# Optimization experiments

Measured on AMD Instinct MI355X. Metric: run time of the kernel, lower is better.

## Reference

```python
import jax, jax.numpy as jnp
import numpy as np

B, T, V, E, H = 128, 512, 32000, 512, 2048


def setup_inputs() -> dict:
    key = jax.random.key(0)
    ks = jax.random.split(key, 10)
    s = lambda k, shape: jax.random.normal(k, shape, dtype=jnp.float32) * 0.02
    return {
        "input_ids": jax.random.randint(ks[0], (B, T), 0, V),
        "emb": s(ks[1], (V, E)),
        # layer 0: embed_size -> hidden_size
        "Wih0": s(ks[2], (H, E)), "Whh0": s(ks[3], (H, H)),
        "bih0": jnp.zeros((H,), jnp.float32), "bhh0": jnp.zeros((H,), jnp.float32),
        # layer 1: hidden_size -> hidden_size
        "Wih1": s(ks[4], (H, H)), "Whh1": s(ks[5], (H, H)),
        "bih1": jnp.zeros((H,), jnp.float32), "bhh1": jnp.zeros((H,), jnp.float32),
        # head: Linear(H,E) -> ReLU -> Linear(E,V)
        "W1": s(ks[6], (E, H)), "b1": jnp.zeros((E,), jnp.float32),
        "W2": s(ks[7], (V, E)), "b2": jnp.zeros((V,), jnp.float32),
    }


def reference(input_ids, emb, Wih0, Whh0, bih0, bhh0, Wih1, Whh1, bih1, bhh1, W1, b1, W2, b2):
    # embedding lookup for whole sequence, then scan over time
    xs = jnp.swapaxes(emb[input_ids], 0, 1)  # [T, B, E]
    b = input_ids.shape[0]
    h_init = (jnp.zeros((b, Whh0.shape[0]), xs.dtype),
              jnp.zeros((b, Whh1.shape[0]), xs.dtype))

    def step(carry, x_t):
        h0, h1 = carry
        h0 = jnp.tanh(x_t @ Wih0.T + bih0 + h0 @ Whh0.T + bhh0)
        h1 = jnp.tanh(h0 @ Wih1.T + bih1 + h1 @ Whh1.T + bhh1)
        return (h0, h1), None

    (_, h1), _ = jax.lax.scan(step, h_init, xs)
    # MLP head on final top-layer hidden state only
    return jnp.maximum(h1 @ W1.T + b1, 0.0) @ W2.T + b2  # [B, V]
```

## Files before the change

kernel.cpp:

```cpp
#include <hip/hip_runtime.h>
#include <hip/hip_bf16.h>
#include <stdint.h>

#define Bn 128
#define Tn 512
#define En 512
#define Hn 2048
#define Vn 32000
#define R0 8
#define R1 4
#define HSLOT (Bn*Hn)

typedef float f32x4 __attribute__((ext_vector_type(4)));
typedef short bf16x8 __attribute__((ext_vector_type(8)));
typedef unsigned long long u64;

__device__ __forceinline__ unsigned short f2b(float f) {
  uint32_t x = __builtin_bit_cast(uint32_t, f);
  uint32_t r = x + 0x7FFFu + ((x >> 16) & 1u);
  return (unsigned short)(r >> 16);
}

union U16x8 { bf16x8 v; u64 q[2]; };
union F32x4u { f32x4 v; u64 q[2]; };

__device__ __forceinline__ bf16x8 ld_h(const unsigned short* p) {
  U16x8 u;
  u.q[0] = __hip_atomic_load((const u64*)p,     __ATOMIC_RELAXED, __HIP_MEMORY_SCOPE_AGENT);
  u.q[1] = __hip_atomic_load((const u64*)p + 1, __ATOMIC_RELAXED, __HIP_MEMORY_SCOPE_AGENT);
  return u.v;
}
__device__ __forceinline__ f32x4 ld_p(const float* p) {
  F32x4u u;
  u.q[0] = __hip_atomic_load((const u64*)p,     __ATOMIC_RELAXED, __HIP_MEMORY_SCOPE_AGENT);
  u.q[1] = __hip_atomic_load((const u64*)p + 1, __ATOMIC_RELAXED, __HIP_MEMORY_SCOPE_AGENT);
  return u.v;
}
__device__ __forceinline__ void st_p(float* p, f32x4 x) {
  F32x4u u; u.v = x;
  __hip_atomic_store((u64*)p,     u.q[0], __ATOMIC_RELAXED, __HIP_MEMORY_SCOPE_AGENT);
  __hip_atomic_store((u64*)p + 1, u.q[1], __ATOMIC_RELAXED, __HIP_MEMORY_SCOPE_AGENT);
}
__device__ __forceinline__ uint32_t ldf(const uint32_t* p) {
  return __hip_atomic_load(p, __ATOMIC_RELAXED, __HIP_MEMORY_SCOPE_AGENT);
}
__device__ __forceinline__ void stf(uint32_t* p, uint32_t v) {
  __hip_atomic_store(p, v, __ATOMIC_RELAXED, __HIP_MEMORY_SCOPE_AGENT);
}
__device__ __forceinline__ void drain_then_sync() {
  asm volatile("s_waitcnt vmcnt(0)" ::: "memory");
  __syncthreads();
}

#define NREP 8
#define FA_PART_BASE 8192
#define FB_PART_BASE 9216
#define FLAG_WORDS 16384


__global__ void zero3(uint32_t* a, int na, uint32_t* b, int nb, uint32_t* c, int nc) {
  int i = blockIdx.x * 256 + threadIdx.x;
  if (i < na) a[i] = 0u;
  if (i < nb) b[i] = 0u;
  if (i < nc) c[i] = 0u;
}

__global__ void pack_bias(const float* bih0, const float* bhh0,
                          const float* bih1, const float* bhh1,
                          float* bias0, float* bias1) {
  int i = blockIdx.x * 256 + threadIdx.x;
  bias0[i] = bih0[i] + bhh0[i];
  bias1[i] = bih1[i] + bhh1[i];
}

__global__ void pack_imgA(const float* __restrict__ Wih0, const float* __restrict__ Whh0,
                          uint4* __restrict__ imgA) {
  int tid = blockIdx.x * 256 + threadIdx.x;
  int wg = tid / 5120;
  int p  = tid - wg * 5120;
  int l = p & 63;
  int ckt = p >> 6;
  int ct = ckt & 3, kt = ckt >> 2;
  int g = wg >> 2, s = wg & 3;
  int col = g * 64 + ct * 16 + (l & 15);
  int kv0 = s * 640 + kt * 32 + (l >> 4) * 8;
  const float* src = (kv0 < 512) ? (Wih0 + (size_t)col * En + kv0)
                                 : (Whh0 + (size_t)col * Hn + (kv0 - 512));
  unsigned short o[8];
#pragma unroll
  for (int j = 0; j < 8; ++j) o[j] = f2b(src[j]);
  imgA[tid] = *reinterpret_cast<uint4*>(o);
}

__global__ void pack_imgB(const float* __restrict__ Wih1, const float* __restrict__ Whh1,
                          uint4* __restrict__ imgB) {
  int tid = blockIdx.x * 256 + threadIdx.x;
  int wg = tid >> 13;
  int p  = tid & 8191;
  int l = p & 63;
  int ckt = p >> 6;
  int ct = ckt & 3, kt = ckt >> 2;
  int g = wg >> 2, s = wg & 3;
  int col = g * 64 + ct * 16 + (l & 15);
  int kv0 = s * 1024 + kt * 32 + (l >> 4) * 8;
  const float* src = (kv0 < 2048) ? (Wih1 + (size_t)col * Hn + kv0)
                                  : (Whh1 + (size_t)col * Hn + (kv0 - 2048));
  unsigned short o[8];
#pragma unroll
  for (int j = 0; j < 8; ++j) o[j] = f2b(src[j]);
  imgB[tid] = *reinterpret_cast<uint4*>(o);
}

__global__ void pack_imgW1(const float* __restrict__ W1, uint4* __restrict__ img) {
  int tid = blockIdx.x * 256 + threadIdx.x;
  int grp = tid >> 12;
  int p = tid & 4095;
  int l = p & 63;
  int kt = p >> 6;
  int col = grp * 16 + (l & 15);
  int k0 = kt * 32 + (l >> 4) * 8;
  const float* src = W1 + (size_t)col * Hn + k0;
  unsigned short o[8];
#pragma unroll
  for (int j = 0; j < 8; ++j) o[j] = f2b(src[j]);
  img[tid] = *reinterpret_cast<uint4*>(o);
}

__global__ void pack_imgW2(const float* __restrict__ W2, uint4* __restrict__ img) {
  int tid = blockIdx.x * 256 + threadIdx.x;
  int grp = tid >> 12;
  int p = tid & 4095;
  int l = p & 63;
  int ckt = p >> 6;
  int ct = ckt & 3, kt = ckt >> 2;
  int col = grp * 64 + ct * 16 + (l & 15);
  int k0 = kt * 32 + (l >> 4) * 8;
  const float* src = W2 + (size_t)col * En + k0;
  unsigned short o[8];
#pragma unroll
  for (int j = 0; j < 8; ++j) o[j] = f2b(src[j]);
  img[tid] = *reinterpret_cast<uint4*>(o);
}

__global__ void gather_x(const int* __restrict__ ids, const float* __restrict__ emb,
                         uint4* __restrict__ xall) {
  int tid = blockIdx.x * 256 + threadIdx.x;
  int t = tid >> 13;
  int r = tid & 8191;
  int b = r >> 6;
  int e8 = r & 63;
  int id = ids[b * Tn + t];
  const float* src = emb + (size_t)id * En + e8 * 8;
  unsigned short o[8];
#pragma unroll
  for (int j = 0; j < 8; ++j) o[j] = f2b(src[j]);
  xall[tid] = *reinterpret_cast<uint4*>(o);
}

__global__ __launch_bounds__(256) void rnn_persist(
    const uint4* __restrict__ imgA, const uint4* __restrict__ imgB,
    const unsigned short* __restrict__ xall,
    unsigned short* __restrict__ h0ring, unsigned short* __restrict__ h1ring,
    float* __restrict__ pbufA, float* __restrict__ pbufB,
    const float* __restrict__ bias0, const float* __restrict__ bias1,
    uint32_t* flags) {
  __shared__ uint4 smem[8192];
  const int tid = threadIdx.x;
  const int w = tid >> 6;
  const int l = tid & 63;
  const int l15 = l & 15;
  const int kq = l >> 4;
  const int blk = blockIdx.x;
  const int myrep = blk & (NREP - 1);
  const uint32_t* fA0r = flags + (size_t)myrep * 1024;
  const uint32_t* fB0r = flags + (size_t)myrep * 1024 + 64;
  uint32_t* fApart = flags + FA_PART_BASE;
  uint32_t* fBpart = flags + FB_PART_BASE;

  const bool roleA = (blk < 128);
  {
    const uint4* src = roleA ? (imgA + (size_t)blk * 5120) : (imgB + (size_t)(blk - 128) * 8192);
    const int n = roleA ? 5120 : 8192;
    for (int i = tid; i < n; i += 256) smem[i] = src[i];
  }
  __syncthreads();
  const bf16x8* wlds = reinterpret_cast<const bf16x8*>(smem);
  const int row0 = w * 32 + l15;

  if (roleA) {
    const int g = blk >> 2, s = blk & 3;
    const int colbase = g * 64;
    for (int t = 0; t < Tn; ++t) {
      {
        const bool ring = (s == 0) && (t + 1 > R0);
        for (;;) {
          int ok = 1;
          if (tid < 32) ok = (ldf(&fA0r[tid]) >= (uint32_t)t);
          if (ring && tid >= 64 && tid < 96)
            ok &= (ldf(&fB0r[tid - 64]) >= (uint32_t)(t + 1 - R0));
          if (__syncthreads_and(ok)) break;
          __builtin_amdgcn_s_sleep(2);
        }
        __builtin_amdgcn_fence(__ATOMIC_ACQUIRE, "workgroup");
      }
      const unsigned short* h0prev = h0ring + (size_t)((t + R0 - 1) % R0) * HSLOT;
      const unsigned short* xt = xall + (size_t)t * (Bn * En);
      f32x4 acc[2][4];
#pragma unroll
      for (int mt = 0; mt < 2; ++mt)
#pragma unroll
        for (int ct = 0; ct < 4; ++ct) acc[mt][ct] = (f32x4){0.f, 0.f, 0.f, 0.f};
#pragma unroll 4
      for (int kt = 0; kt < 20; ++kt) {
        const int kv = s * 640 + kt * 32;
        bf16x8 af0, af1;
        if (kv < 512) {
          af0 = *reinterpret_cast<const bf16x8*>(xt + kv + (size_t)row0 * En + kq * 8);
          af1 = *reinterpret_cast<const bf16x8*>(xt + kv + (size_t)(row0 + 16) * En + kq * 8);
        } else {
          const unsigned short* hp = h0prev + (kv - 512);
          af0 = ld_h(hp + (size_t)row0 * Hn + kq * 8);
          af1 = ld_h(hp + (size_t)(row0 + 16) * Hn + kq * 8);
        }
#pragma unroll
        for (int ct = 0; ct < 4; ++ct) {
          bf16x8 bf = wlds[(kt * 4 + ct) * 64 + l];
          acc[0][ct] = __builtin_amdgcn_mfma_f32_16x16x32_bf16(af0, bf, acc[0][ct], 0, 0, 0);
          acc[1][ct] = __builtin_amdgcn_mfma_f32_16x16x32_bf16(af1, bf, acc[1][ct], 0, 0, 0);
        }
      }
      if (s != 0) {
        float* slot = pbufA + (size_t)blk * 8192;
#pragma unroll
        for (int mt = 0; mt < 2; ++mt)
#pragma unroll
          for (int ct = 0; ct < 4; ++ct)
            st_p(slot + ((w * 8 + mt * 4 + ct) * 256 + l * 4), acc[mt][ct]);
        drain_then_sync();
        if (tid == 0) stf(&fApart[g * 16 + s], (uint32_t)(t + 1));
      } else {
        for (;;) {
          int ok = 1;
          if (tid < 3) ok = (ldf(&fApart[g * 16 + 1 + tid]) >= (uint32_t)(t + 1));
          if (__syncthreads_and(ok)) break;
          __builtin_amdgcn_s_sleep(2);
        }
        __builtin_amdgcn_fence(__ATOMIC_ACQUIRE, "workgroup");
        const float* p1 = pbufA + (size_t)(blk + 1) * 8192;
        const float* p2 = pbufA + (size_t)(blk + 2) * 8192;
        const float* p3 = pbufA + (size_t)(blk + 3) * 8192;
        unsigned short* h0cur = h0ring + (size_t)(t % R0) * HSLOT;
#pragma unroll
        for (int mt = 0; mt < 2; ++mt) {
#pragma unroll
          for (int ct = 0; ct < 4; ++ct) {
            const int base = (w * 8 + mt * 4 + ct) * 256 + l * 4;
            f32x4 sum = acc[mt][ct];
            sum += ld_p(p1 + base);
            sum += ld_p(p2 + base);
            sum += ld_p(p3 + base);
            const int col = colbase + ct * 16 + l15;
            const float bb = bias0[col];
#pragma unroll
            for (int r = 0; r < 4; ++r) {
              float v = tanhf(sum[r] + bb);
              int bo = f2b(v);
              int po = __shfl_down(bo, 1);
              if ((l15 & 1) == 0) {
                const int row = w * 32 + mt * 16 + kq * 4 + r;
                uint32_t packed = (uint32_t)(unsigned short)bo | ((uint32_t)(unsigned short)po << 16);
                stf((uint32_t*)(h0cur + (size_t)row * Hn + col), packed);
              }
            }
          }
        }
        drain_then_sync();
        if (tid < NREP) stf(flags + (size_t)tid * 1024 + g, (uint32_t)(t + 1));
      }
    }
  } else {
    const int bb = blk - 128;
    const int g = bb >> 2, s = bb & 3;
    const int colbase = g * 64;
    for (int t = 0; t < Tn; ++t) {
      {
        const bool ring = (s == 0) && (t + 2 > R1);
        for (;;) {
          int ok = 1;
          if (s < 2) {
            if (tid < 32) ok = (ldf(&fA0r[tid]) >= (uint32_t)(t + 1));
            if (s == 1 && t > 0 && tid == 33)
              ok &= (ldf(&fB0r[g]) >= (uint32_t)t);
          } else {
            if (tid < 32) ok = (ldf(&fB0r[tid]) >= (uint32_t)t);
          }
          if (ring && tid >= 64 && tid < 96)
            ok &= (ldf(&fB0r[tid - 64]) >= (uint32_t)(t + 2 - R1));
          if (__syncthreads_and(ok)) break;
          __builtin_amdgcn_s_sleep(2);
        }
        __builtin_amdgcn_fence(__ATOMIC_ACQUIRE, "workgroup");
      }
      const unsigned short* h0cur = h0ring + (size_t)(t % R0) * HSLOT;
      const unsigned short* h1prev = h1ring + (size_t)((t + R1 - 1) % R1) * HSLOT;
      const unsigned short* apbase;
      if (s == 0)      apbase = h0cur;
      else if (s == 1) apbase = h0cur + 1024;
      else if (s == 2) apbase = h1prev;
      else             apbase = h1prev + 1024;
      f32x4 acc[2][4];
#pragma unroll
      for (int mt = 0; mt < 2; ++mt)
#pragma unroll
        for (int ct = 0; ct < 4; ++ct) acc[mt][ct] = (f32x4){0.f, 0.f, 0.f, 0.f};
#pragma unroll 4
      for (int kt = 0; kt < 32; ++kt) {
        const unsigned short* ap = apbase + kt * 32;
        bf16x8 af0 = ld_h(ap + (size_t)row0 * Hn + kq * 8);
        bf16x8 af1 = ld_h(ap + (size_t)(row0 + 16) * Hn + kq * 8);
#pragma unroll
        for (int ct = 0; ct < 4; ++ct) {
          bf16x8 bf = wlds[(kt * 4 + ct) * 64 + l];
          acc[0][ct] = __builtin_amdgcn_mfma_f32_16x16x32_bf16(af0, bf, acc[0][ct], 0, 0, 0);
          acc[1][ct] = __builtin_amdgcn_mfma_f32_16x16x32_bf16(af1, bf, acc[1][ct], 0, 0, 0);
        }
      }
      if (s != 0) {
        float* slot = pbufB + (size_t)bb * 8192;
#pragma unroll
        for (int mt = 0; mt < 2; ++mt)
#pragma unroll
          for (int ct = 0; ct < 4; ++ct)
            st_p(slot + ((w * 8 + mt * 4 + ct) * 256 + l * 4), acc[mt][ct]);
        drain_then_sync();
        if (tid == 0) stf(&fBpart[g * 16 + s], (uint32_t)(t + 1));
      } else {
        for (;;) {
          int ok = 1;
          if (tid < 3) ok = (ldf(&fBpart[g * 16 + 1 + tid]) >= (uint32_t)(t + 1));
          if (__syncthreads_and(ok)) break;
          __builtin_amdgcn_s_sleep(2);
        }
        __builtin_amdgcn_fence(__ATOMIC_ACQUIRE, "workgroup");
        const float* p1 = pbufB + (size_t)(bb + 1) * 8192;
        const float* p2 = pbufB + (size_t)(bb + 2) * 8192;
        const float* p3 = pbufB + (size_t)(bb + 3) * 8192;
        unsigned short* h1cur = h1ring + (size_t)(t % R1) * HSLOT;
#pragma unroll
        for (int mt = 0; mt < 2; ++mt) {
#pragma unroll
          for (int ct = 0; ct < 4; ++ct) {
            const int base = (w * 8 + mt * 4 + ct) * 256 + l * 4;
            f32x4 sum = acc[mt][ct];
            sum += ld_p(p1 + base);
            sum += ld_p(p2 + base);
            sum += ld_p(p3 + base);
            const int col = colbase + ct * 16 + l15;
            const float bb2 = bias1[col];
#pragma unroll
            for (int r = 0; r < 4; ++r) {
              float v = tanhf(sum[r] + bb2);
              int bo = f2b(v);
              int po = __shfl_down(bo, 1);
              if ((l15 & 1) == 0) {
                const int row = w * 32 + mt * 16 + kq * 4 + r;
                uint32_t packed = (uint32_t)(unsigned short)bo | ((uint32_t)(unsigned short)po << 16);
                stf((uint32_t*)(h1cur + (size_t)row * Hn + col), packed);
              }
            }
          }
        }
        drain_then_sync();
        if (tid < NREP) stf(flags + (size_t)tid * 1024 + 64 + g, (uint32_t)(t + 1));
      }
    }
  }
}

__global__ __launch_bounds__(256) void head1(const uint4* __restrict__ imgW1,
                                             const unsigned short* __restrict__ h1f,
                                             const float* __restrict__ b1,
                                             unsigned short* __restrict__ a1) {
  __shared__ uint4 smem[4096];
  const int tid = threadIdx.x;
  const int w = tid >> 6, l = tid & 63, l15 = l & 15, kq = l >> 4;
  const int g = blockIdx.x;
  const uint4* src = imgW1 + (size_t)g * 4096;
  for (int i = tid; i < 4096; i += 256) smem[i] = src[i];
  __syncthreads();
  const bf16x8* wlds = reinterpret_cast<const bf16x8*>(smem);
  const int row0 = w * 32 + l15;
  f32x4 acc[2];
  acc[0] = (f32x4){0.f, 0.f, 0.f, 0.f};
  acc[1] = (f32x4){0.f, 0.f, 0.f, 0.f};
#pragma unroll 4
  for (int kt = 0; kt < 64; ++kt) {
    bf16x8 af0 = *reinterpret_cast<const bf16x8*>(h1f + (size_t)row0 * Hn + kt * 32 + kq * 8);
    bf16x8 af1 = *reinterpret_cast<const bf16x8*>(h1f + (size_t)(row0 + 16) * Hn + kt * 32 + kq * 8);
    bf16x8 bf = wlds[kt * 64 + l];
    acc[0] = __builtin_amdgcn_mfma_f32_16x16x32_bf16(af0, bf, acc[0], 0, 0, 0);
    acc[1] = __builtin_amdgcn_mfma_f32_16x16x32_bf16(af1, bf, acc[1], 0, 0, 0);
  }
  const int col = g * 16 + l15;
  const float bb = b1[col];
#pragma unroll
  for (int mt = 0; mt < 2; ++mt)
#pragma unroll
    for (int r = 0; r < 4; ++r) {
      float v = fmaxf(acc[mt][r] + bb, 0.f);
      const int row = w * 32 + mt * 16 + kq * 4 + r;
      a1[(size_t)row * En + col] = f2b(v);
    }
}

__global__ __launch_bounds__(256) void head2(const uint4* __restrict__ imgW2,
                                             const unsigned short* __restrict__ a1,
                                             const float* __restrict__ b2,
                                             float* __restrict__ out) {
  __shared__ uint4 smem[4096];
  const int tid = threadIdx.x;
  const int w = tid >> 6, l = tid & 63, l15 = l & 15, kq = l >> 4;
  const int g = blockIdx.x;
  const uint4* src = imgW2 + (size_t)g * 4096;
  for (int i = tid; i < 4096; i += 256) smem[i] = src[i];
  __syncthreads();
  const bf16x8* wlds = reinterpret_cast<const bf16x8*>(smem);
  const int row0 = w * 32 + l15;
  f32x4 acc[2][4];
#pragma unroll
  for (int mt = 0; mt < 2; ++mt)
#pragma unroll
    for (int ct = 0; ct < 4; ++ct) acc[mt][ct] = (f32x4){0.f, 0.f, 0.f, 0.f};
#pragma unroll
  for (int kt = 0; kt < 16; ++kt) {
    bf16x8 af0 = *reinterpret_cast<const bf16x8*>(a1 + (size_t)row0 * En + kt * 32 + kq * 8);
    bf16x8 af1 = *reinterpret_cast<const bf16x8*>(a1 + (size_t)(row0 + 16) * En + kt * 32 + kq * 8);
#pragma unroll
    for (int ct = 0; ct < 4; ++ct) {
      bf16x8 bf = wlds[(kt * 4 + ct) * 64 + l];
      acc[0][ct] = __builtin_amdgcn_mfma_f32_16x16x32_bf16(af0, bf, acc[0][ct], 0, 0, 0);
      acc[1][ct] = __builtin_amdgcn_mfma_f32_16x16x32_bf16(af1, bf, acc[1][ct], 0, 0, 0);
    }
  }
#pragma unroll
  for (int mt = 0; mt < 2; ++mt)
#pragma unroll
    for (int ct = 0; ct < 4; ++ct) {
      const int col = g * 64 + ct * 16 + l15;
      const float bb = b2[col];
#pragma unroll
      for (int r = 0; r < 4; ++r) {
        const int row = w * 32 + mt * 16 + kq * 4 + r;
        out[(size_t)row * Vn + col] = acc[mt][ct][r] + bb;
      }
    }
}

extern "C" void kernel_launch(void* const* d_in, const int* in_sizes, int n_in,
                              void* d_out, int out_size, void* d_ws, size_t ws_size,
                              hipStream_t stream) {
  (void)in_sizes; (void)n_in; (void)out_size;
  const int* ids    = (const int*)d_in[0];
  const float* emb  = (const float*)d_in[1];
  const float* Wih0 = (const float*)d_in[2];
  const float* Whh0 = (const float*)d_in[3];
  const float* bih0 = (const float*)d_in[4];
  const float* bhh0 = (const float*)d_in[5];
  const float* Wih1 = (const float*)d_in[6];
  const float* Whh1 = (const float*)d_in[7];
  const float* bih1 = (const float*)d_in[8];
  const float* bhh1 = (const float*)d_in[9];
  const float* W1   = (const float*)d_in[10];
  const float* b1   = (const float*)d_in[11];
  const float* W2   = (const float*)d_in[12];
  const float* b2   = (const float*)d_in[13];
  float* out = (float*)d_out;

  char* ws = (char*)d_ws;
  size_t o = 0;
  auto alloc = [&](size_t bytes) -> char* {
    char* p = ws + o;
    o += (bytes + 255) & ~(size_t)255;
    return p;
  };
  uint32_t* flags = (uint32_t*)alloc(FLAG_WORDS * 4);
  float* bias0 = (float*)alloc(Hn * 4);
  float* bias1 = (float*)alloc(Hn * 4);
  unsigned short* h0ring = (unsigned short*)alloc((size_t)R0 * HSLOT * 2);
  unsigned short* h1ring = (unsigned short*)alloc((size_t)R1 * HSLOT * 2);
  float* pbufA = (float*)alloc(128ull * 8192 * 4);
  float* pbufB = (float*)alloc(128ull * 8192 * 4);
  unsigned short* a1 = (unsigned short*)alloc((size_t)Bn * En * 2);
  uint4* imgA  = (uint4*)alloc(128ull * 5120 * 16);
  uint4* imgB  = (uint4*)alloc(128ull * 8192 * 16);
  uint4* imgW1 = (uint4*)alloc(32ull * 4096 * 16);
  uint4* imgW2 = (uint4*)alloc(500ull * 4096 * 16);
  uint4* xall  = (uint4*)alloc((size_t)Tn * Bn * En * 2);
  if (o > ws_size) return;

  zero3<<<512, 256, 0, stream>>>(flags, FLAG_WORDS,
                                 (uint32_t*)(h0ring + (size_t)(R0 - 1) * HSLOT), 131072,
                                 (uint32_t*)(h1ring + (size_t)(R1 - 1) * HSLOT), 131072);
  pack_bias<<<8, 256, 0, stream>>>(bih0, bhh0, bih1, bhh1, bias0, bias1);
  pack_imgA<<<2560, 256, 0, stream>>>(Wih0, Whh0, imgA);
  pack_imgB<<<4096, 256, 0, stream>>>(Wih1, Whh1, imgB);
  pack_imgW1<<<512, 256, 0, stream>>>(W1, imgW1);
  pack_imgW2<<<8000, 256, 0, stream>>>(W2, imgW2);
  gather_x<<<16384, 256, 0, stream>>>(ids, emb, xall);

  rnn_persist<<<256, 256, 0, stream>>>(imgA, imgB, (const unsigned short*)xall,
                                       h0ring, h1ring, pbufA, pbufB, bias0, bias1, flags);

  head1<<<32, 256, 0, stream>>>(imgW1, h1ring + (size_t)(511 % R1) * HSLOT, b1, a1);
  head2<<<500, 256, 0, stream>>>(imgW2, a1, b2, out);
}
```

Baseline: 14.10 ms.

## Split RNN into four weight roles with in-block K-split and off-critical-path input projections

The persistent RNN kernel is restructured into four roles of 64 blocks each (Whh0, Wih0, Wih1, Whh1), each owning 32 output columns with 512 threads. The two halves of each block split K and reduce through LDS instead of through cross-block partial buffers. The x·Wih0 and h1·Whh1 products are computed ahead of time by separate blocks into double-buffered partials, which shortens the serial dependency chain per timestep. Activation loads become batched inline-asm global loads with cache-bypass bits. The cost is more complex flag dependencies and a risk of deadlock or ordering bugs.

```diff
diff --git a/kernel.cpp b/kernel.cpp
--- a/kernel.cpp
+++ b/kernel.cpp
@@ -11,6 +11,10 @@
 #define R1 4
 #define HSLOT (Bn*Hn)
 
+#define NREP 8
+#define FXS 8192
+#define FLAG_WORDS 16384
+
 typedef float f32x4 __attribute__((ext_vector_type(4)));
 typedef short bf16x8 __attribute__((ext_vector_type(8)));
 typedef unsigned long long u64;
@@ -21,15 +25,7 @@
   return (unsigned short)(r >> 16);
 }
 
-union U16x8 { bf16x8 v; u64 q[2]; };
 union F32x4u { f32x4 v; u64 q[2]; };
-
-__device__ __forceinline__ bf16x8 ld_h(const unsigned short* p) {
-  U16x8 u;
-  u.q[0] = __hip_atomic_load((const u64*)p,     __ATOMIC_RELAXED, __HIP_MEMORY_SCOPE_AGENT);
-  u.q[1] = __hip_atomic_load((const u64*)p + 1, __ATOMIC_RELAXED, __HIP_MEMORY_SCOPE_AGENT);
-  return u.v;
-}
 __device__ __forceinline__ f32x4 ld_p(const float* p) {
   F32x4u u;
   u.q[0] = __hip_atomic_load((const u64*)p,     __ATOMIC_RELAXED, __HIP_MEMORY_SCOPE_AGENT);
@@ -51,11 +47,6 @@
   asm volatile("s_waitcnt vmcnt(0)" ::: "memory");
   __syncthreads();
 }
-
-#define NREP 8
-#define FA_PART_BASE 8192
-#define FB_PART_BASE 9216
-#define FLAG_WORDS 16384
 
 
 __global__ void zero3(uint32_t* a, int na, uint32_t* b, int nb, uint32_t* c, int nc) {
@@ -73,42 +64,19 @@
   bias1[i] = bih1[i] + bhh1[i];
 }
 
-__global__ void pack_imgA(const float* __restrict__ Wih0, const float* __restrict__ Whh0,
-                          uint4* __restrict__ imgA) {
+__global__ void pack_w32(const float* __restrict__ src, int Kd, uint4* __restrict__ img) {
   int tid = blockIdx.x * 256 + threadIdx.x;
-  int wg = tid / 5120;
-  int p  = tid - wg * 5120;
-  int l = p & 63;
-  int ckt = p >> 6;
-  int ct = ckt & 3, kt = ckt >> 2;
-  int g = wg >> 2, s = wg & 3;
-  int col = g * 64 + ct * 16 + (l & 15);
-  int kv0 = s * 640 + kt * 32 + (l >> 4) * 8;
-  const float* src = (kv0 < 512) ? (Wih0 + (size_t)col * En + kv0)
-                                 : (Whh0 + (size_t)col * Hn + (kv0 - 512));
+  int per = Kd * 4;
+  int g = tid / per, p = tid - g * per;
+  int l = p & 63, q = p >> 6;
+  int ct = q & 1, kt = q >> 1;
+  int col = g * 32 + ct * 16 + (l & 15);
+  int k0 = kt * 32 + (l >> 4) * 8;
+  const float* s = src + (size_t)col * Kd + k0;
   unsigned short o[8];
 #pragma unroll
-  for (int j = 0; j < 8; ++j) o[j] = f2b(src[j]);
-  imgA[tid] = *reinterpret_cast<uint4*>(o);
-}
-
-__global__ void pack_imgB(const float* __restrict__ Wih1, const float* __restrict__ Whh1,
-                          uint4* __restrict__ imgB) {
-  int tid = blockIdx.x * 256 + threadIdx.x;
-  int wg = tid >> 13;
-  int p  = tid & 8191;
-  int l = p & 63;
-  int ckt = p >> 6;
-  int ct = ckt & 3, kt = ckt >> 2;
-  int g = wg >> 2, s = wg & 3;
-  int col = g * 64 + ct * 16 + (l & 15);
-  int kv0 = s * 1024 + kt * 32 + (l >> 4) * 8;
-  const float* src = (kv0 < 2048) ? (Wih1 + (size_t)col * Hn + kv0)
-                                  : (Whh1 + (size_t)col * Hn + (kv0 - 2048));
-  unsigned short o[8];
-#pragma unroll
-  for (int j = 0; j < 8; ++j) o[j] = f2b(src[j]);
-  imgB[tid] = *reinterpret_cast<uint4*>(o);
+  for (int j = 0; j < 8; ++j) o[j] = f2b(s[j]);
+  img[tid] = *reinterpret_cast<uint4*>(o);
 }
 
 __global__ void pack_imgW1(const float* __restrict__ W1, uint4* __restrict__ img) {
@@ -157,223 +125,195 @@
   xall[tid] = *reinterpret_cast<uint4*>(o);
 }
 
-__global__ __launch_bounds__(256) void rnn_persist(
-    const uint4* __restrict__ imgA, const uint4* __restrict__ imgB,
+__global__ __launch_bounds__(512, 1) void rnn_persist(
+    const uint4* __restrict__ imgWhh0, const uint4* __restrict__ imgWih0,
+    const uint4* __restrict__ imgWih1, const uint4* __restrict__ imgWhh1,
     const unsigned short* __restrict__ xall,
     unsigned short* __restrict__ h0ring, unsigned short* __restrict__ h1ring,
-    float* __restrict__ pbufA, float* __restrict__ pbufB,
+    float* __restrict__ xpbuf, float* __restrict__ bpbuf,
     const float* __restrict__ bias0, const float* __restrict__ bias1,
     uint32_t* flags) {
   __shared__ uint4 smem[8192];
+  __shared__ f32x4 rbuf[1024];
   const int tid = threadIdx.x;
-  const int w = tid >> 6;
-  const int l = tid & 63;
-  const int l15 = l & 15;
-  const int kq = l >> 4;
+  const int w = tid >> 6, l = tid & 63, l15 = l & 15, kq = l >> 4;
+  const int wh = w & 3, half = w >> 2;
   const int blk = blockIdx.x;
+  const int role = blk >> 6, g = blk & 63;
   const int myrep = blk & (NREP - 1);
   const uint32_t* fA0r = flags + (size_t)myrep * 1024;
-  const uint32_t* fB0r = flags + (size_t)myrep * 1024 + 64;
-  uint32_t* fApart = flags + FA_PART_BASE;
-  uint32_t* fBpart = flags + FB_PART_BASE;
-
-  const bool roleA = (blk < 128);
-  {
-    const uint4* src = roleA ? (imgA + (size_t)blk * 5120) : (imgB + (size_t)(blk - 128) * 8192);
-    const int n = roleA ? 5120 : 8192;
-    for (int i = tid; i < n; i += 256) smem[i] = src[i];
-  }
+  const uint32_t* fB0r = flags + (size_t)myrep * 1024 + 128;
+  const uint32_t* fP1r = flags + (size_t)myrep * 1024 + 256;
+
+  const uint4* wsrc; int npkt, Kd;
+  if (role == 0)      { wsrc = imgWhh0 + (size_t)g * 8192; npkt = 8192; Kd = 2048; }
+  else if (role == 1) { wsrc = imgWih0 + (size_t)g * 2048; npkt = 2048; Kd = 512; }
+  else if (role == 2) { wsrc = imgWih1 + (size_t)g * 8192; npkt = 8192; Kd = 2048; }
+  else                { wsrc = imgWhh1 + (size_t)g * 8192; npkt = 8192; Kd = 2048; }
+  for (int i = tid; i < npkt; i += 512) smem[i] = wsrc[i];
   __syncthreads();
   const bf16x8* wlds = reinterpret_cast<const bf16x8*>(smem);
-  const int row0 = w * 32 + l15;
-
-  if (roleA) {
-    const int g = blk >> 2, s = blk & 3;
-    const int colbase = g * 64;
-    for (int t = 0; t < Tn; ++t) {
-      {
-        const bool ring = (s == 0) && (t + 1 > R0);
+  const int row0 = wh * 32 + l15;
+  const int nb = Kd >> 9;
+  const int khe = half * (Kd >> 1);
+  const int kt0 = khe >> 5;
+
+  for (int t = 0; t < Tn; ++t) {
+    if (role == 0) {
+      const bool ring = (t + 1 > R0);
+      for (;;) {
+        int ok = 1;
+        if (tid < 64) ok = (ldf(&fA0r[tid]) >= (uint32_t)t);
+        else if (tid == 64) ok = (ldf(flags + FXS + g * 16) >= (uint32_t)(t + 1));
+        else if (ring && tid >= 128 && tid < 192) ok = (ldf(&fB0r[tid - 128]) >= (uint32_t)(t + 1 - R0));
+        if (__syncthreads_and(ok)) break;
+        __builtin_amdgcn_s_sleep(1);
+      }
+    } else if (role == 1) {
+      if (t >= 2) {
         for (;;) {
           int ok = 1;
-          if (tid < 32) ok = (ldf(&fA0r[tid]) >= (uint32_t)t);
-          if (ring && tid >= 64 && tid < 96)
-            ok &= (ldf(&fB0r[tid - 64]) >= (uint32_t)(t + 1 - R0));
+          if (tid == 0) ok = (ldf(&fA0r[g]) >= (uint32_t)(t - 1));
           if (__syncthreads_and(ok)) break;
           __builtin_amdgcn_s_sleep(2);
         }
-        __builtin_amdgcn_fence(__ATOMIC_ACQUIRE, "workgroup");
-      }
-      const unsigned short* h0prev = h0ring + (size_t)((t + R0 - 1) % R0) * HSLOT;
-      const unsigned short* xt = xall + (size_t)t * (Bn * En);
-      f32x4 acc[2][4];
+      }
+    } else if (role == 2) {
+      const bool ring = (t + 2 > R1);
+      for (;;) {
+        int ok = 1;
+        if (tid < 64) ok = (ldf(&fA0r[tid]) >= (uint32_t)(t + 1));
+        else if (tid == 64) ok = (ldf(&fP1r[g]) >= (uint32_t)(t + 1));
+        else if (ring && tid >= 128 && tid < 192) ok = (ldf(&fP1r[tid - 128]) >= (uint32_t)(t + 2 - R1));
+        if (__syncthreads_and(ok)) break;
+        __builtin_amdgcn_s_sleep(1);
+      }
+    } else {
+      for (;;) {
+        int ok = 1;
+        if (tid < 64) ok = (ldf(&fB0r[tid]) >= (uint32_t)t);
+        if (__syncthreads_and(ok)) break;
+        __builtin_amdgcn_s_sleep(1);
+      }
+    }
+    __builtin_amdgcn_fence(__ATOMIC_ACQUIRE, "workgroup");
+
+    const unsigned short* asrc; int astride;
+    if (role == 0)      { asrc = h0ring + (size_t)((t + R0 - 1) % R0) * HSLOT; astride = Hn; }
+    else if (role == 1) { asrc = xall + (size_t)t * (Bn * En); astride = En; }
+    else if (role == 2) { asrc = h0ring + (size_t)(t % R0) * HSLOT; astride = Hn; }
+    else                { asrc = h1ring + (size_t)((t + R1 - 1) % R1) * HSLOT; astride = Hn; }
+
+    f32x4 acc[2][2];
+#pragma unroll
+    for (int mt = 0; mt < 2; ++mt)
+#pragma unroll
+      for (int ct = 0; ct < 2; ++ct) acc[mt][ct] = (f32x4){0.f, 0.f, 0.f, 0.f};
+
+    const unsigned short* pr0 = asrc + (size_t)row0 * astride + khe + kq * 8;
+    const unsigned short* pr1 = pr0 + (size_t)16 * astride;
+    for (int b = 0; b < nb; ++b) {
+      const unsigned short* pa = pr0 + b * 256;
+      const unsigned short* pb = pr1 + b * 256;
+      bf16x8 v0, v1, v2, v3, v4, v5, v6, v7, v8, v9, va, vb, vc, vd, ve, vf;
+      asm volatile(
+          "global_load_dwordx4 %[t0], %[a], off sc0 sc1\n\t"
+          "global_load_dwordx4 %[t1], %[a], off offset:64 sc0 sc1\n\t"
+          "global_load_dwordx4 %[t2], %[a], off offset:128 sc0 sc1\n\t"
+          "global_load_dwordx4 %[t3], %[a], off offset:192 sc0 sc1\n\t"
+          "global_load_dwordx4 %[t4], %[a], off offset:256 sc0 sc1\n\t"
+          "global_load_dwordx4 %[t5], %[a], off offset:320 sc0 sc1\n\t"
+          "global_load_dwordx4 %[t6], %[a], off offset:384 sc0 sc1\n\t"
+          "global_load_dwordx4 %[t7], %[a], off offset:448 sc0 sc1\n\t"
+          "global_load_dwordx4 %[t8], %[b], off sc0 sc1\n\t"
+          "global_load_dwordx4 %[t9], %[b], off offset:64 sc0 sc1\n\t"
+          "global_load_dwordx4 %[ta], %[b], off offset:128 sc0 sc1\n\t"
+          "global_load_dwordx4 %[tb], %[b], off offset:192 sc0 sc1\n\t"
+          "global_load_dwordx4 %[tc], %[b], off offset:256 sc0 sc1\n\t"
+          "global_load_dwordx4 %[td], %[b], off offset:320 sc0 sc1\n\t"
+          "global_load_dwordx4 %[te], %[b], off offset:384 sc0 sc1\n\t"
+          "global_load_dwordx4 %[tf], %[b], off offset:448 sc0 sc1\n\t"
+          "s_waitcnt vmcnt(0)"
+          : [t0]"=&v"(v0), [t1]"=&v"(v1), [t2]"=&v"(v2), [t3]"=&v"(v3),
+            [t4]"=&v"(v4), [t5]"=&v"(v5), [t6]"=&v"(v6), [t7]"=&v"(v7),
+            [t8]"=&v"(v8), [t9]"=&v"(v9), [ta]"=&v"(va), [tb]"=&v"(vb),
+            [tc]"=&v"(vc), [td]"=&v"(vd), [te]"=&v"(ve), [tf]"=&v"(vf)
+          : [a]"v"(pa), [b]"v"(pb)
+          : "memory");
+      __builtin_amdgcn_sched_barrier(0);
+      const int ktg = kt0 + b * 8;
+#define MFMA4(AF0, AF1, KT) do { \
+        bf16x8 bw0 = wlds[((KT) * 2) * 64 + l]; \
+        bf16x8 bw1 = wlds[((KT) * 2 + 1) * 64 + l]; \
+        acc[0][0] = __builtin_amdgcn_mfma_f32_16x16x32_bf16(AF0, bw0, acc[0][0], 0, 0, 0); \
+        acc[0][1] = __builtin_amdgcn_mfma_f32_16x16x32_bf16(AF0, bw1, acc[0][1], 0, 0, 0); \
+        acc[1][0] = __builtin_amdgcn_mfma_f32_16x16x32_bf16(AF1, bw0, acc[1][0], 0, 0, 0); \
+        acc[1][1] = __builtin_amdgcn_mfma_f32_16x16x32_bf16(AF1, bw1, acc[1][1], 0, 0, 0); \
+      } while (0)
+      MFMA4(v0, v8, ktg + 0); MFMA4(v1, v9, ktg + 1);
+      MFMA4(v2, va, ktg + 2); MFMA4(v3, vb, ktg + 3);
+      MFMA4(v4, vc, ktg + 4); MFMA4(v5, vd, ktg + 5);
+      MFMA4(v6, ve, ktg + 6); MFMA4(v7, vf, ktg + 7);
+#undef MFMA4
+    }
+
+    __syncthreads();
+    if (half == 1) {
 #pragma unroll
       for (int mt = 0; mt < 2; ++mt)
 #pragma unroll
-        for (int ct = 0; ct < 4; ++ct) acc[mt][ct] = (f32x4){0.f, 0.f, 0.f, 0.f};
-#pragma unroll 4
-      for (int kt = 0; kt < 20; ++kt) {
-        const int kv = s * 640 + kt * 32;
-        bf16x8 af0, af1;
-        if (kv < 512) {
-          af0 = *reinterpret_cast<const bf16x8*>(xt + kv + (size_t)row0 * En + kq * 8);
-          af1 = *reinterpret_cast<const bf16x8*>(xt + kv + (size_t)(row0 + 16) * En + kq * 8);
-        } else {
-          const unsigned short* hp = h0prev + (kv - 512);
-          af0 = ld_h(hp + (size_t)row0 * Hn + kq * 8);
-          af1 = ld_h(hp + (size_t)(row0 + 16) * Hn + kq * 8);
-        }
-#pragma unroll
-        for (int ct = 0; ct < 4; ++ct) {
-          bf16x8 bf = wlds[(kt * 4 + ct) * 64 + l];
-          acc[0][ct] = __builtin_amdgcn_mfma_f32_16x16x32_bf16(af0, bf, acc[0][ct], 0, 0, 0);
-          acc[1][ct] = __builtin_amdgcn_mfma_f32_16x16x32_bf16(af1, bf, acc[1][ct], 0, 0, 0);
-        }
-      }
-      if (s != 0) {
-        float* slot = pbufA + (size_t)blk * 8192;
-#pragma unroll
-        for (int mt = 0; mt < 2; ++mt)
-#pragma unroll
-          for (int ct = 0; ct < 4; ++ct)
-            st_p(slot + ((w * 8 + mt * 4 + ct) * 256 + l * 4), acc[mt][ct]);
-        drain_then_sync();
-        if (tid == 0) stf(&fApart[g * 16 + s], (uint32_t)(t + 1));
-      } else {
-        for (;;) {
-          int ok = 1;
-          if (tid < 3) ok = (ldf(&fApart[g * 16 + 1 + tid]) >= (uint32_t)(t + 1));
-          if (__syncthreads_and(ok)) break;
-          __builtin_amdgcn_s_sleep(2);
-        }
-        __builtin_amdgcn_fence(__ATOMIC_ACQUIRE, "workgroup");
-        const float* p1 = pbufA + (size_t)(blk + 1) * 8192;
-        const float* p2 = pbufA + (size_t)(blk + 2) * 8192;
-        const float* p3 = pbufA + (size_t)(blk + 3) * 8192;
-        unsigned short* h0cur = h0ring + (size_t)(t % R0) * HSLOT;
+        for (int ct = 0; ct < 2; ++ct)
+          rbuf[(wh * 4 + mt * 2 + ct) * 64 + l] = acc[mt][ct];
+    }
+    __syncthreads();
+
+    if (half == 0) {
+#pragma unroll
+      for (int mt = 0; mt < 2; ++mt)
+#pragma unroll
+        for (int ct = 0; ct < 2; ++ct)
+          acc[mt][ct] += rbuf[(wh * 4 + mt * 2 + ct) * 64 + l];
+
+      if (role == 0 || role == 2) {
+        const float* pb2 = (role == 0 ? xpbuf : bpbuf) + (size_t)(g * 2 + (t & 1)) * 4096;
+        const float* bsrc = (role == 0) ? bias0 : bias1;
+        unsigned short* hdst = (role == 0) ? (h0ring + (size_t)(t % R0) * HSLOT)
+                                           : (h1ring + (size_t)(t % R1) * HSLOT);
 #pragma unroll
         for (int mt = 0; mt < 2; ++mt) {
 #pragma unroll
-          for (int ct = 0; ct < 4; ++ct) {
-            const int base = (w * 8 + mt * 4 + ct) * 256 + l * 4;
-            f32x4 sum = acc[mt][ct];
-            sum += ld_p(p1 + base);
-            sum += ld_p(p2 + base);
-            sum += ld_p(p3 + base);
-            const int col = colbase + ct * 16 + l15;
-            const float bb = bias0[col];
+          for (int ct = 0; ct < 2; ++ct) {
+            const int idx = (wh * 4 + mt * 2 + ct) * 256 + l * 4;
+            f32x4 sum = acc[mt][ct] + ld_p(pb2 + idx);
+            const int col = g * 32 + ct * 16 + l15;
+            const float bb = bsrc[col];
 #pragma unroll
             for (int r = 0; r < 4; ++r) {
               float v = tanhf(sum[r] + bb);
               int bo = f2b(v);
               int po = __shfl_down(bo, 1);
               if ((l15 & 1) == 0) {
-                const int row = w * 32 + mt * 16 + kq * 4 + r;
+                const int row = wh * 32 + mt * 16 + kq * 4 + r;
                 uint32_t packed = (uint32_t)(unsigned short)bo | ((uint32_t)(unsigned short)po << 16);
-                stf((uint32_t*)(h0cur + (size_t)row * Hn + col), packed);
+                stf((uint32_t*)(hdst + (size_t)row * Hn + col), packed);
               }
             }
           }
         }
-        drain_then_sync();
-        if (tid < NREP) stf(flags + (size_t)tid * 1024 + g, (uint32_t)(t + 1));
-      }
-    }
-  } else {
-    const int bb = blk - 128;
-    const int g = bb >> 2, s = bb & 3;
-    const int colbase = g * 64;
-    for (int t = 0; t < Tn; ++t) {
-      {
-        const bool ring = (s == 0) && (t + 2 > R1);
-        for (;;) {
-          int ok = 1;
-          if (s < 2) {
-            if (tid < 32) ok = (ldf(&fA0r[tid]) >= (uint32_t)(t + 1));
-            if (s == 1 && t > 0 && tid == 33)
-              ok &= (ldf(&fB0r[g]) >= (uint32_t)t);
-          } else {
-            if (tid < 32) ok = (ldf(&fB0r[tid]) >= (uint32_t)t);
-          }
-          if (ring && tid >= 64 && tid < 96)
-            ok &= (ldf(&fB0r[tid - 64]) >= (uint32_t)(t + 2 - R1));
-          if (__syncthreads_and(ok)) break;
-          __builtin_amdgcn_s_sleep(2);
-        }
-        __builtin_amdgcn_fence(__ATOMIC_ACQUIRE, "workgroup");
-      }
-      const unsigned short* h0cur = h0ring + (size_t)(t % R0) * HSLOT;
-      const unsigned short* h1prev = h1ring + (size_t)((t + R1 - 1) % R1) * HSLOT;
-      const unsigned short* apbase;
-      if (s == 0)      apbase = h0cur;
-      else if (s == 1) apbase = h0cur + 1024;
-      else if (s == 2) apbase = h1prev;
-      else             apbase = h1prev + 1024;
-      f32x4 acc[2][4];
-#pragma unroll
-      for (int mt = 0; mt < 2; ++mt)
-#pragma unroll
-        for (int ct = 0; ct < 4; ++ct) acc[mt][ct] = (f32x4){0.f, 0.f, 0.f, 0.f};
-#pragma unroll 4
-      for (int kt = 0; kt < 32; ++kt) {
-        const unsigned short* ap = apbase + kt * 32;
-        bf16x8 af0 = ld_h(ap + (size_t)row0 * Hn + kq * 8);
-        bf16x8 af1 = ld_h(ap + (size_t)(row0 + 16) * Hn + kq * 8);
-#pragma unroll
-        for (int ct = 0; ct < 4; ++ct) {
-          bf16x8 bf = wlds[(kt * 4 + ct) * 64 + l];
-          acc[0][ct] = __builtin_amdgcn_mfma_f32_16x16x32_bf16(af0, bf, acc[0][ct], 0, 0, 0);
-          acc[1][ct] = __builtin_amdgcn_mfma_f32_16x16x32_bf16(af1, bf, acc[1][ct], 0, 0, 0);
-        }
-      }
-      if (s != 0) {
-        float* slot = pbufB + (size_t)bb * 8192;
+      } else {
+        float* dst = (role == 1 ? xpbuf : bpbuf) + (size_t)(g * 2 + (t & 1)) * 4096;
 #pragma unroll
         for (int mt = 0; mt < 2; ++mt)
 #pragma unroll
-          for (int ct = 0; ct < 4; ++ct)
-            st_p(slot + ((w * 8 + mt * 4 + ct) * 256 + l * 4), acc[mt][ct]);
-        drain_then_sync();
-        if (tid == 0) stf(&fBpart[g * 16 + s], (uint32_t)(t + 1));
-      } else {
-        for (;;) {
-          int ok = 1;
-          if (tid < 3) ok = (ldf(&fBpart[g * 16 + 1 + tid]) >= (uint32_t)(t + 1));
-          if (__syncthreads_and(ok)) break;
-          __builtin_amdgcn_s_sleep(2);
-        }
-        __builtin_amdgcn_fence(__ATOMIC_ACQUIRE, "workgroup");
-        const float* p1 = pbufB + (size_t)(bb + 1) * 8192;
-        const float* p2 = pbufB + (size_t)(bb + 2) * 8192;
-        const float* p3 = pbufB + (size_t)(bb + 3) * 8192;
-        unsigned short* h1cur = h1ring + (size_t)(t % R1) * HSLOT;
-#pragma unroll
-        for (int mt = 0; mt < 2; ++mt) {
-#pragma unroll
-          for (int ct = 0; ct < 4; ++ct) {
-            const int base = (w * 8 + mt * 4 + ct) * 256 + l * 4;
-            f32x4 sum = acc[mt][ct];
-            sum += ld_p(p1 + base);
-            sum += ld_p(p2 + base);
-            sum += ld_p(p3 + base);
-            const int col = colbase + ct * 16 + l15;
-            const float bb2 = bias1[col];
-#pragma unroll
-            for (int r = 0; r < 4; ++r) {
-              float v = tanhf(sum[r] + bb2);
-              int bo = f2b(v);
-              int po = __shfl_down(bo, 1);
-              if ((l15 & 1) == 0) {
-                const int row = w * 32 + mt * 16 + kq * 4 + r;
-                uint32_t packed = (uint32_t)(unsigned short)bo | ((uint32_t)(unsigned short)po << 16);
-                stf((uint32_t*)(h1cur + (size_t)row * Hn + col), packed);
-              }
-            }
-          }
-        }
-        drain_then_sync();
-        if (tid < NREP) stf(flags + (size_t)tid * 1024 + 64 + g, (uint32_t)(t + 1));
-      }
-    }
+          for (int ct = 0; ct < 2; ++ct)
+            st_p(dst + (wh * 4 + mt * 2 + ct) * 256 + l * 4, acc[mt][ct]);
+      }
+    }
+    drain_then_sync();
+    if (role == 0)      { if (tid < NREP) stf(flags + (size_t)tid * 1024 + g, (uint32_t)(t + 1)); }
+    else if (role == 1) { if (tid == 0) stf(flags + FXS + g * 16, (uint32_t)(t + 1)); }
+    else if (role == 2) { if (tid < NREP) stf(flags + (size_t)tid * 1024 + 128 + g, (uint32_t)(t + 1)); }
+    else                { if (tid < NREP) stf(flags + (size_t)tid * 1024 + 256 + g, (uint32_t)(t + 1)); }
   }
 }
 
@@ -488,11 +428,13 @@
   float* bias1 = (float*)alloc(Hn * 4);
   unsigned short* h0ring = (unsigned short*)alloc((size_t)R0 * HSLOT * 2);
   unsigned short* h1ring = (unsigned short*)alloc((size_t)R1 * HSLOT * 2);
-  float* pbufA = (float*)alloc(128ull * 8192 * 4);
-  float* pbufB = (float*)alloc(128ull * 8192 * 4);
+  float* xpbuf = (float*)alloc(64ull * 2 * 4096 * 4);
+  float* bpbuf = (float*)alloc(64ull * 2 * 4096 * 4);
   unsigned short* a1 = (unsigned short*)alloc((size_t)Bn * En * 2);
-  uint4* imgA  = (uint4*)alloc(128ull * 5120 * 16);
-  uint4* imgB  = (uint4*)alloc(128ull * 8192 * 16);
+  uint4* imgWhh0 = (uint4*)alloc(64ull * 8192 * 16);
+  uint4* imgWih0 = (uint4*)alloc(64ull * 2048 * 16);
+  uint4* imgWih1 = (uint4*)alloc(64ull * 8192 * 16);
+  uint4* imgWhh1 = (uint4*)alloc(64ull * 8192 * 16);
   uint4* imgW1 = (uint4*)alloc(32ull * 4096 * 16);
   uint4* imgW2 = (uint4*)alloc(500ull * 4096 * 16);
   uint4* xall  = (uint4*)alloc((size_t)Tn * Bn * En * 2);
@@ -502,14 +444,17 @@
                                  (uint32_t*)(h0ring + (size_t)(R0 - 1) * HSLOT), 131072,
                                  (uint32_t*)(h1ring + (size_t)(R1 - 1) * HSLOT), 131072);
   pack_bias<<<8, 256, 0, stream>>>(bih0, bhh0, bih1, bhh1, bias0, bias1);
-  pack_imgA<<<2560, 256, 0, stream>>>(Wih0, Whh0, imgA);
-  pack_imgB<<<4096, 256, 0, stream>>>(Wih1, Whh1, imgB);
+  pack_w32<<<2048, 256, 0, stream>>>(Whh0, 2048, imgWhh0);
+  pack_w32<<<512, 256, 0, stream>>>(Wih0, 512, imgWih0);
+  pack_w32<<<2048, 256, 0, stream>>>(Wih1, 2048, imgWih1);
+  pack_w32<<<2048, 256, 0, stream>>>(Whh1, 2048, imgWhh1);
   pack_imgW1<<<512, 256, 0, stream>>>(W1, imgW1);
   pack_imgW2<<<8000, 256, 0, stream>>>(W2, imgW2);
   gather_x<<<16384, 256, 0, stream>>>(ids, emb, xall);
 
-  rnn_persist<<<256, 256, 0, stream>>>(imgA, imgB, (const unsigned short*)xall,
-                                       h0ring, h1ring, pbufA, pbufB, bias0, bias1, flags);
+  rnn_persist<<<256, 512, 0, stream>>>(imgWhh0, imgWih0, imgWih1, imgWhh1,
+                                       (const unsigned short*)xall, h0ring, h1ring,
+                                       xpbuf, bpbuf, bias0, bias1, flags);
 
   head1<<<32, 256, 0, stream>>>(imgW1, h1ring + (size_t)(511 % R1) * HSLOT, b1, a1);
   head2<<<500, 256, 0, stream>>>(imgW2, a1, b2, out);
```

Result: slower. 19.48 ms (+38.1%).
